# Optimization experiments

Hardware: AMD Instinct MI355X
Metric: run time of the kernel (lower is better)

Reference implementation:

```python
import jax, jax.numpy as jnp
import numpy as np

B, N = 64, 32768

def setup_inputs() -> dict:
    key = jax.random.key(0)
    k1, k2, k3, k4 = jax.random.split(key, 4)
    audio = jax.random.normal(k1, (B, N), dtype=jnp.float32)
    g = jax.random.uniform(k2, (B, N, 1), dtype=jnp.float32)
    twoR = jax.random.uniform(k3, (B, N, 1), dtype=jnp.float32)
    mix = jax.random.uniform(k4, (B, N, 3), dtype=jnp.float32)
    return {"audio": audio, "g": g, "twoR": twoR, "mix": mix}


def _svf(audio, g, twoR, mix):
    b, n = audio.shape
    T = 1.0 / (1.0 + g * (g + twoR))                      # [B,N,1]
    ones = jnp.ones_like(g)
    # H: [B,N,2,2] time-varying state matrix
    H = T[..., None] * jnp.concatenate(
        [ones, -g, g, twoR * g + 1.0], axis=-1).reshape(b, n, 2, 2)
    gHB = (g * T) * jnp.concatenate([ones, g], axis=-1)   # [B,N,2]
    gHBx = gHB * audio[..., None]                          # [B,N,2]

    # Linear time-varying recurrence: Y_t = gHBx_t + H_t @ s_{t-1}; s_t = 2 Y_t - s_{t-1}
    def step(state, inp):
        Ht, ut = inp                                       # [B,2,2], [B,2]
        Yt = ut + jnp.einsum('bij,bj->bi', Ht, state)
        return 2.0 * Yt - state, Yt

    s0 = jnp.ones((b, 2), dtype=audio.dtype)
    _, Y = jax.lax.scan(step,
                        s0,
                        (jnp.moveaxis(H, 1, 0), jnp.moveaxis(gHBx, 1, 0)))
    Y = jnp.moveaxis(Y, 0, 1)                              # [B,N,2]

    twoR_ = twoR[..., 0]                                   # [B,N]
    y_bp, y_lp = Y[..., 0], Y[..., 1]
    y_hp = audio - twoR_ * y_bp - y_lp
    y_mixed = twoR_ * mix[..., 0] * y_bp + mix[..., 1] * y_lp + mix[..., 2] * y_hp
    return y_mixed


def reference(audio, g, twoR, mix):
    return _svf(audio, g, twoR, mix)
```

## Files before the change

### kernel.cpp

```cpp
#include <hip/hip_runtime.h>


#define BATCH     64
#define SEQ       32768
#define CHUNKS    32
#define CHUNK_LEN (SEQ / CHUNKS)
#define TPB       256
#define NWAVE     (TPB / 64)
#define STEPS     (CHUNK_LEN / TPB)
#define NBLK      (BATCH * CHUNKS)

struct Aff { float a00, a01, a10, a11, b0, b1; };

__device__ __forceinline__ Aff aff_ident() {
    Aff r; r.a00 = 1.f; r.a01 = 0.f; r.a10 = 0.f; r.a11 = 1.f; r.b0 = 0.f; r.b1 = 0.f;
    return r;
}

__device__ __forceinline__ Aff compose(const Aff l, const Aff e) {
    Aff r;
    r.a00 = fmaf(l.a00, e.a00, l.a01 * e.a10);
    r.a01 = fmaf(l.a00, e.a01, l.a01 * e.a11);
    r.a10 = fmaf(l.a10, e.a00, l.a11 * e.a10);
    r.a11 = fmaf(l.a10, e.a01, l.a11 * e.a11);
    r.b0  = fmaf(l.a00, e.b0, fmaf(l.a01, e.b1, l.b0));
    r.b1  = fmaf(l.a10, e.b0, fmaf(l.a11, e.b1, l.b1));
    return r;
}

__device__ __forceinline__ Aff step_affine(float gi, float Ri, float xi) {
    float T  = 1.0f / fmaf(gi, gi + Ri, 1.0f);
    float Tg = T * gi;
    Aff r;
    r.a00 = 2.0f * T - 1.0f;
    r.a01 = -2.0f * Tg;
    r.a10 = 2.0f * Tg;
    r.a11 = 2.0f * fmaf(Tg, Ri, T) - 1.0f;
    r.b0  = 2.0f * Tg * xi;
    r.b1  = gi * r.b0;
    return r;
}

__device__ __forceinline__ Aff shfl_up_aff(const Aff v, int d) {
    Aff r;
    r.a00 = __shfl_up(v.a00, d); r.a01 = __shfl_up(v.a01, d);
    r.a10 = __shfl_up(v.a10, d); r.a11 = __shfl_up(v.a11, d);
    r.b0  = __shfl_up(v.b0,  d); r.b1  = __shfl_up(v.b1,  d);
    return r;
}

__device__ __forceinline__ Aff wave_scan_incl(Aff v, int lane) {
#pragma unroll
    for (int off = 1; off < 64; off <<= 1) {
        Aff p = shfl_up_aff(v, off);
        if (lane >= off) v = compose(v, p);
    }
    return v;
}

__device__ __forceinline__ Aff local_affine(const float gv[4], const float rv[4],
                                            const float xv[4]) {
    Aff a = step_affine(gv[0], rv[0], xv[0]);
#pragma unroll
    for (int i = 1; i < STEPS; ++i)
        a = compose(step_affine(gv[i], rv[i], xv[i]), a);
    return a;
}

__global__ __launch_bounds__(TPB, 4) void svf_k1(
    const float* __restrict__ audio, const float* __restrict__ g,
    const float* __restrict__ twoR, float* __restrict__ agg)
{
    __shared__ Aff wtot[NWAVE];
    const int blk  = blockIdx.x;
    const int t    = threadIdx.x;
    const int lane = t & 63, wave = t >> 6;
    const int base = blk * CHUNK_LEN + t * STEPS;

    float4 g4 = *reinterpret_cast<const float4*>(g + base);
    float4 r4 = *reinterpret_cast<const float4*>(twoR + base);
    float4 x4 = *reinterpret_cast<const float4*>(audio + base);
    float gv[4] = {g4.x, g4.y, g4.z, g4.w};
    float rv[4] = {r4.x, r4.y, r4.z, r4.w};
    float xv[4] = {x4.x, x4.y, x4.z, x4.w};

    Aff W = wave_scan_incl(local_affine(gv, rv, xv), lane);
    if (lane == 63) wtot[wave] = W;
    __syncthreads();

    if (t == TPB - 1) {
        Aff A = wtot[0];
#pragma unroll
        for (int w = 1; w < NWAVE; ++w) A = compose(wtot[w], A);
        float* dst = agg + 6 * blk;
        dst[0] = A.a00; dst[1] = A.a01; dst[2] = A.a10;
        dst[3] = A.a11; dst[4] = A.b0;  dst[5] = A.b1;
    }
}

__global__ __launch_bounds__(TPB, 4) void svf_k2(
    const float* __restrict__ audio, const float* __restrict__ g,
    const float* __restrict__ twoR, const float* __restrict__ mix,
    const float* __restrict__ agg, float* __restrict__ out)
{
    __shared__ Aff wtot[NWAVE];
    __shared__ float csb[2];
    const int blk  = blockIdx.x;
    const int c    = blk & (CHUNKS - 1);
    const int t    = threadIdx.x;
    const int lane = t & 63, wave = t >> 6;
    const int base = blk * CHUNK_LEN + t * STEPS;

    float4 g4 = *reinterpret_cast<const float4*>(g + base);
    float4 r4 = *reinterpret_cast<const float4*>(twoR + base);
    float4 x4 = *reinterpret_cast<const float4*>(audio + base);
    float gv[4] = {g4.x, g4.y, g4.z, g4.w};
    float rv[4] = {r4.x, r4.y, r4.z, r4.w};
    float xv[4] = {x4.x, x4.y, x4.z, x4.w};

    const float4* m4 = reinterpret_cast<const float4*>(mix + 3 * base);
    float4 m0 = m4[0], m1 = m4[1], m2 = m4[2];
    float mv[12] = {m0.x, m0.y, m0.z, m0.w, m1.x, m1.y,
                    m1.z, m1.w, m2.x, m2.y, m2.z, m2.w};

    Aff W = wave_scan_incl(local_affine(gv, rv, xv), lane);
    if (lane == 63) wtot[wave] = W;

    if (wave == 0) {
        Aff p = aff_ident();
        if (lane < c) {
            const float* s = agg + 6 * (blk - c + lane);
            p.a00 = s[0]; p.a01 = s[1]; p.a10 = s[2];
            p.a11 = s[3]; p.b0  = s[4]; p.b1  = s[5];
        }
        p = wave_scan_incl(p, lane);
        const int src = (c > 0) ? (c - 1) : 0;
        if (lane == src) {
            csb[0] = p.a00 + p.a01 + p.b0;
            csb[1] = p.a10 + p.a11 + p.b1;
        }
    }
    __syncthreads();

    const float cs0 = csb[0], cs1 = csb[1];

    Aff P = aff_ident();
    for (int wj = 0; wj < wave; ++wj) P = compose(wtot[wj], P);

    Aff Wp = shfl_up_aff(W, 1);
    Aff E = (lane == 0) ? P : compose(Wp, P);

    float s0 = fmaf(E.a00, cs0, fmaf(E.a01, cs1, E.b0));
    float s1 = fmaf(E.a10, cs0, fmaf(E.a11, cs1, E.b1));

    float ov[STEPS];
#pragma unroll
    for (int i = 0; i < STEPS; ++i) {
        float gi = gv[i], Ri = rv[i], xi = xv[i];
        float T  = 1.0f / fmaf(gi, gi + Ri, 1.0f);
        float w  = fmaf(gi, xi, s0);
        float Y0 = T * fmaf(-gi, s1, w);
        float Y1 = T * fmaf(gi, w, fmaf(Ri, gi, 1.0f) * s1);
        float hp = xi - Ri * Y0 - Y1;
        ov[i] = fmaf(Ri * mv[3*i], Y0, fmaf(mv[3*i+1], Y1, mv[3*i+2] * hp));
        s0 = fmaf(2.0f, Y0, -s0);
        s1 = fmaf(2.0f, Y1, -s1);
    }

    *reinterpret_cast<float4*>(out + base) = make_float4(ov[0], ov[1], ov[2], ov[3]);
}

extern "C" void kernel_launch(void* const* d_in, const int* in_sizes, int n_in,
                              void* d_out, int out_size, void* d_ws, size_t ws_size,
                              hipStream_t stream) {
    const float* audio = (const float*)d_in[0];
    const float* g     = (const float*)d_in[1];
    const float* twoR  = (const float*)d_in[2];
    const float* mix   = (const float*)d_in[3];
    float* out = (float*)d_out;
    float* agg = (float*)d_ws;

    svf_k1<<<NBLK, TPB, 0, stream>>>(audio, g, twoR, agg);
    svf_k2<<<NBLK, TPB, 0, stream>>>(audio, g, twoR, mix, agg, out);
}
```

Baseline: 97.19 us.

## Fuse two-pass chunk scan into single kernel with flag-based decoupled lookback

Merges the aggregate pass and the apply pass into one kernel. Each block publishes its chunk affine aggregate to workspace with a release flag, and later blocks spin on the flags of earlier chunks in the same batch row. This removes the second read of g, twoR and audio and one kernel launch. It also halves the chunk count so each thread handles 8 samples. The cost is a memset of the flags, spin-waiting that relies on earlier blocks being scheduled first, and a longer serial per-thread chain.

```diff
diff --git a/kernel.cpp b/kernel.cpp
--- a/kernel.cpp
+++ b/kernel.cpp
@@ -3,7 +3,7 @@
 
 #define BATCH     64
 #define SEQ       32768
-#define CHUNKS    32
+#define CHUNKS    16
 #define CHUNK_LEN (SEQ / CHUNKS)
 #define TPB       256
 #define NWAVE     (TPB / 64)
@@ -58,50 +58,17 @@
     return v;
 }
 
-__device__ __forceinline__ Aff local_affine(const float gv[4], const float rv[4],
-                                            const float xv[4]) {
-    Aff a = step_affine(gv[0], rv[0], xv[0]);
-#pragma unroll
-    for (int i = 1; i < STEPS; ++i)
-        a = compose(step_affine(gv[i], rv[i], xv[i]), a);
-    return a;
+__device__ __forceinline__ void load8(const float* __restrict__ p, int base, float v[8]) {
+    float4 a = *reinterpret_cast<const float4*>(p + base);
+    float4 b = *reinterpret_cast<const float4*>(p + base + 4);
+    v[0]=a.x; v[1]=a.y; v[2]=a.z; v[3]=a.w; v[4]=b.x; v[5]=b.y; v[6]=b.z; v[7]=b.w;
 }
 
-__global__ __launch_bounds__(TPB, 4) void svf_k1(
-    const float* __restrict__ audio, const float* __restrict__ g,
-    const float* __restrict__ twoR, float* __restrict__ agg)
-{
-    __shared__ Aff wtot[NWAVE];
-    const int blk  = blockIdx.x;
-    const int t    = threadIdx.x;
-    const int lane = t & 63, wave = t >> 6;
-    const int base = blk * CHUNK_LEN + t * STEPS;
-
-    float4 g4 = *reinterpret_cast<const float4*>(g + base);
-    float4 r4 = *reinterpret_cast<const float4*>(twoR + base);
-    float4 x4 = *reinterpret_cast<const float4*>(audio + base);
-    float gv[4] = {g4.x, g4.y, g4.z, g4.w};
-    float rv[4] = {r4.x, r4.y, r4.z, r4.w};
-    float xv[4] = {x4.x, x4.y, x4.z, x4.w};
-
-    Aff W = wave_scan_incl(local_affine(gv, rv, xv), lane);
-    if (lane == 63) wtot[wave] = W;
-    __syncthreads();
-
-    if (t == TPB - 1) {
-        Aff A = wtot[0];
-#pragma unroll
-        for (int w = 1; w < NWAVE; ++w) A = compose(wtot[w], A);
-        float* dst = agg + 6 * blk;
-        dst[0] = A.a00; dst[1] = A.a01; dst[2] = A.a10;
-        dst[3] = A.a11; dst[4] = A.b0;  dst[5] = A.b1;
-    }
-}
-
-__global__ __launch_bounds__(TPB, 4) void svf_k2(
+__global__ __launch_bounds__(TPB, 4) void svf_fused2(
     const float* __restrict__ audio, const float* __restrict__ g,
     const float* __restrict__ twoR, const float* __restrict__ mix,
-    const float* __restrict__ agg, float* __restrict__ out)
+    float* __restrict__ agg, int* __restrict__ flags,
+    float* __restrict__ out)
 {
     __shared__ Aff wtot[NWAVE];
     __shared__ float csb[2];
@@ -111,27 +78,52 @@
     const int lane = t & 63, wave = t >> 6;
     const int base = blk * CHUNK_LEN + t * STEPS;
 
-    float4 g4 = *reinterpret_cast<const float4*>(g + base);
-    float4 r4 = *reinterpret_cast<const float4*>(twoR + base);
-    float4 x4 = *reinterpret_cast<const float4*>(audio + base);
-    float gv[4] = {g4.x, g4.y, g4.z, g4.w};
-    float rv[4] = {r4.x, r4.y, r4.z, r4.w};
-    float xv[4] = {x4.x, x4.y, x4.z, x4.w};
+    float gv[STEPS], rv[STEPS], xv[STEPS];
+    load8(g, base, gv); load8(twoR, base, rv); load8(audio, base, xv);
 
     const float4* m4 = reinterpret_cast<const float4*>(mix + 3 * base);
-    float4 m0 = m4[0], m1 = m4[1], m2 = m4[2];
-    float mv[12] = {m0.x, m0.y, m0.z, m0.w, m1.x, m1.y,
-                    m1.z, m1.w, m2.x, m2.y, m2.z, m2.w};
+    float mv[24];
+#pragma unroll
+    for (int q = 0; q < 6; ++q) {
+        float4 m = m4[q];
+        mv[4*q+0]=m.x; mv[4*q+1]=m.y; mv[4*q+2]=m.z; mv[4*q+3]=m.w;
+    }
 
-    Aff W = wave_scan_incl(local_affine(gv, rv, xv), lane);
+    Aff acc = step_affine(gv[0], rv[0], xv[0]);
+#pragma unroll
+    for (int i = 1; i < STEPS; ++i)
+        acc = compose(step_affine(gv[i], rv[i], xv[i]), acc);
+    Aff W = wave_scan_incl(acc, lane);
     if (lane == 63) wtot[wave] = W;
+    __syncthreads();
+
+    if (t == TPB - 1 && c != CHUNKS - 1) {
+        Aff A = wtot[0];
+#pragma unroll
+        for (int w = 1; w < NWAVE; ++w) A = compose(wtot[w], A);
+        float* dst = agg + 6 * blk;
+        const float* s = (const float*)&A;
+#pragma unroll
+        for (int k = 0; k < 6; ++k)
+            __hip_atomic_store(dst + k, s[k], __ATOMIC_RELAXED, __HIP_MEMORY_SCOPE_AGENT);
+        __hip_atomic_store(&flags[blk], 1, __ATOMIC_RELEASE, __HIP_MEMORY_SCOPE_AGENT);
+    }
 
     if (wave == 0) {
+        const int pb = blk - c + lane;
+        if (lane < c) {
+            while (__hip_atomic_load(&flags[pb], __ATOMIC_RELAXED,
+                                     __HIP_MEMORY_SCOPE_AGENT) == 0)
+                __builtin_amdgcn_s_sleep(16);
+        }
+        __builtin_amdgcn_fence(__ATOMIC_ACQUIRE, "agent");
         Aff p = aff_ident();
         if (lane < c) {
-            const float* s = agg + 6 * (blk - c + lane);
-            p.a00 = s[0]; p.a01 = s[1]; p.a10 = s[2];
-            p.a11 = s[3]; p.b0  = s[4]; p.b1  = s[5];
+            const float* s = agg + 6 * pb;
+#pragma unroll
+            for (int k = 0; k < 6; ++k)
+                ((float*)&p)[k] = __hip_atomic_load(s + k, __ATOMIC_RELAXED,
+                                                    __HIP_MEMORY_SCOPE_AGENT);
         }
         p = wave_scan_incl(p, lane);
         const int src = (c > 0) ? (c - 1) : 0;
@@ -167,7 +159,8 @@
         s1 = fmaf(2.0f, Y1, -s1);
     }
 
-    *reinterpret_cast<float4*>(out + base) = make_float4(ov[0], ov[1], ov[2], ov[3]);
+    *reinterpret_cast<float4*>(out + base)     = make_float4(ov[0], ov[1], ov[2], ov[3]);
+    *reinterpret_cast<float4*>(out + base + 4) = make_float4(ov[4], ov[5], ov[6], ov[7]);
 }
 
 extern "C" void kernel_launch(void* const* d_in, const int* in_sizes, int n_in,
@@ -178,8 +171,10 @@
     const float* twoR  = (const float*)d_in[2];
     const float* mix   = (const float*)d_in[3];
     float* out = (float*)d_out;
-    float* agg = (float*)d_ws;
 
-    svf_k1<<<NBLK, TPB, 0, stream>>>(audio, g, twoR, agg);
-    svf_k2<<<NBLK, TPB, 0, stream>>>(audio, g, twoR, mix, agg, out);
+    float* agg   = (float*)d_ws;
+    int*   flags = (int*)((char*)d_ws + NBLK * sizeof(Aff));
+
+    hipMemsetAsync(flags, 0, NBLK * sizeof(int), stream);
+    svf_fused2<<<NBLK, TPB, 0, stream>>>(audio, g, twoR, mix, agg, flags, out);
 }
```

Result: slower. 144.2 us (+48.4%).
